# Kernel optimization log

Measured on AMD Instinct MI355X. Metric: run time of the kernel, lower is better.

Reference implementation:

```python
import jax, jax.numpy as jnp
import numpy as np

D_MODEL = 512
INF = 1e9
TEMP = np.sqrt(D_MODEL).astype(np.float32)


def setup_inputs() -> dict:
    key = jax.random.key(0)
    kq, kk, kv, km = jax.random.split(key, 4)
    B, L, D = 64, 1024, 64  # B = batch*heads
    q = jax.random.normal(kq, (B, L, D), dtype=jnp.float32)
    k = jax.random.normal(kk, (B, L, D), dtype=jnp.float32)
    v = jax.random.normal(kv, (B, L, D), dtype=jnp.float32)
    attn_mask = jax.random.randint(km, (B, L, L), 0, 2).astype(jnp.bool_)
    return {"q": q, "k": k, "v": v, "attn_mask": attn_mask}


def reference(q, k, v, attn_mask):
    # scores: [b, len_q, len_k]
    attn = jnp.einsum('bqd,bkd->bqk', q, k) / TEMP
    attn = jnp.where(attn_mask, -INF, attn)
    attn = jax.nn.softmax(attn, axis=2)
    # dropout p=0.0 -> identity
    out = jnp.einsum('bqk,bkd->bqd', attn, v)
    return out
```

## Files before the change

### kernel.cpp

```cpp
#include <hip/hip_runtime.h>
#include <hip/hip_bf16.h>


typedef __attribute__((ext_vector_type(4))) float f32x4;
typedef __attribute__((ext_vector_type(8))) short bf16x8;
typedef __attribute__((ext_vector_type(4))) short short4v;

constexpr int B_ = 64;
constexpr int L_ = 1024;
constexpr int D_ = 64;
constexpr int QBLK = 64;
constexpr int KV = 64;
constexpr int NKV = L_ / KV;
constexpr int STR = 72;
constexpr float INV_TEMP = 0.04419417382415922f;
constexpr float NEG = -1e9f;

__device__ inline short f2bf(float f) {
  __hip_bfloat16 h = __float2bfloat16(f);
  short s; __builtin_memcpy(&s, &h, 2);
  return s;
}

__global__ __launch_bounds__(256, 3) void attn_fwd(
    const float* __restrict__ Q, const float* __restrict__ K,
    const float* __restrict__ V, const int* __restrict__ M,
    float* __restrict__ O)
{
  __shared__ short k_lds[2][KV][STR];
  __shared__ short vt_lds[2][D_][STR];
  __shared__ short p_lds[4][16][STR];

  const int tid  = threadIdx.x;
  const int w    = tid >> 6;
  const int lane = tid & 63;
  const int g    = lane >> 4;
  const int c    = lane & 15;

  const int p   = blockIdx.x;
  const int xcd = p & 7;
  const int j   = p >> 3;
  const int b   = xcd + 8 * (j >> 4);
  const int q0  = (j & 15) * QBLK;

  bf16x8 qf[2];
  {
    const float* qp = Q + ((size_t)b * L_ + q0 + w * 16 + c) * D_ + g * 8;
#pragma unroll
    for (int ks = 0; ks < 2; ++ks) {
      f32x4 x0 = *(const f32x4*)(qp + ks * 32);
      f32x4 x1 = *(const f32x4*)(qp + ks * 32 + 4);
      bf16x8 t;
      t[0] = f2bf(x0[0] * INV_TEMP); t[1] = f2bf(x0[1] * INV_TEMP);
      t[2] = f2bf(x0[2] * INV_TEMP); t[3] = f2bf(x0[3] * INV_TEMP);
      t[4] = f2bf(x1[0] * INV_TEMP); t[5] = f2bf(x1[1] * INV_TEMP);
      t[6] = f2bf(x1[2] * INV_TEMP); t[7] = f2bf(x1[3] * INV_TEMP);
      qf[ks] = t;
    }
  }

  const float* Kb = K + (size_t)b * L_ * D_;
  const float* Vb = V + (size_t)b * L_ * D_;
  const int* mlane = M + (size_t)b * L_ * L_ + (size_t)(q0 + w * 16 + c) * L_ + 4 * g;

  f32x4 kreg[4], vreg[4];
  int4  mA[4], mB[4];
  const int vkey4 = (tid & 15) * 4;
  const int vd4   = (tid >> 4) * 4;

  auto load_kv = [&](int t) {
    const float* ksrc = Kb + (size_t)(t * KV) * D_;
    const float* vsrc = Vb + (size_t)(t * KV) * D_;
#pragma unroll
    for (int i = 0; i < 4; ++i) {
      kreg[i] = *(const f32x4*)(ksrc + (size_t)(tid + i * 256) * 4);
      vreg[i] = *(const f32x4*)(vsrc + (size_t)(vkey4 + i) * D_ + vd4);
    }
  };
  auto load_m = [&](int t, int4 (&mr)[4]) {
#pragma unroll
    for (int f = 0; f < 4; ++f) mr[f] = *(const int4*)(mlane + t * KV + f * 16);
  };
  auto write_kv = [&](int buf) {
#pragma unroll
    for (int i = 0; i < 4; ++i) {
      const int idx = tid + i * 256;
      short4v ks4 = { f2bf(kreg[i][0]), f2bf(kreg[i][1]),
                      f2bf(kreg[i][2]), f2bf(kreg[i][3]) };
      *(short4v*)&k_lds[buf][idx >> 4][(idx & 15) * 4] = ks4;
      const int jj = (i + (tid >> 4)) & 3;
      short4v vt4 = { f2bf(vreg[0][jj]), f2bf(vreg[1][jj]),
                      f2bf(vreg[2][jj]), f2bf(vreg[3][jj]) };
      *(short4v*)&vt_lds[buf][vd4 + jj][vkey4] = vt4;
    }
  };

  f32x4 acc[4];
#pragma unroll
  for (int i = 0; i < 4; ++i) acc[i] = (f32x4){0.f, 0.f, 0.f, 0.f};
  float m_run = -INFINITY;
  float l_run = 0.f;

  load_kv(0);
  write_kv(0);
  load_m(0, mA);
  load_m(1, mB);
  __syncthreads();

  auto body = [&](int t, int4 (&mbuf)[4], bool refill) {
    const int cur = t & 1;
    const bool has_next = (t + 1 < NKV);
    if (has_next) load_kv(t + 1);
    int4 mc[4];
#pragma unroll
    for (int f = 0; f < 4; ++f) mc[f] = mbuf[f];
    if (refill) load_m(t + 2, mbuf);
    __builtin_amdgcn_sched_barrier(0);

    f32x4 sc[4];
#pragma unroll
    for (int f = 0; f < 4; ++f) {
      const int4 mm = mc[f];
      sc[f][0] = mm.x ? NEG : 0.0f;
      sc[f][1] = mm.y ? NEG : 0.0f;
      sc[f][2] = mm.z ? NEG : 0.0f;
      sc[f][3] = mm.w ? NEG : 0.0f;
    }

#pragma unroll
    for (int f = 0; f < 4; ++f) {
      f32x4 a = sc[f];
#pragma unroll
      for (int ks = 0; ks < 2; ++ks) {
        bf16x8 kf = *(const bf16x8*)&k_lds[cur][f * 16 + c][ks * 32 + g * 8];
        a = __builtin_amdgcn_mfma_f32_16x16x32_bf16(kf, qf[ks], a, 0, 0, 0);
      }
      sc[f] = a;
    }

    float x = sc[0][0];
#pragma unroll
    for (int f = 0; f < 4; ++f)
#pragma unroll
      for (int r = 0; r < 4; ++r) x = fmaxf(x, sc[f][r]);
    x = fmaxf(x, __shfl_xor(x, 16, 64));
    x = fmaxf(x, __shfl_xor(x, 32, 64));
    const float m_new = fmaxf(m_run, x);
    const float alpha = __expf(m_run - m_new);
    float s = 0.f;
#pragma unroll
    for (int f = 0; f < 4; ++f)
#pragma unroll
      for (int r = 0; r < 4; ++r) {
        sc[f][r] = __expf(sc[f][r] - m_new);
        s += sc[f][r];
      }
    s += __shfl_xor(s, 16, 64);
    s += __shfl_xor(s, 32, 64);
    l_run = l_run * alpha + s;
    m_run = m_new;

    float ar[4];
#pragma unroll
    for (int r = 0; r < 4; ++r)
      ar[r] = __shfl(alpha, (lane & 48) | (g * 4 + r), 64);
#pragma unroll
    for (int fd = 0; fd < 4; ++fd)
#pragma unroll
      for (int r = 0; r < 4; ++r) acc[fd][r] *= ar[r];

#pragma unroll
    for (int f = 0; f < 4; ++f) {
      short4v pk = { f2bf(sc[f][0]), f2bf(sc[f][1]),
                     f2bf(sc[f][2]), f2bf(sc[f][3]) };
      *(short4v*)&p_lds[w][c][f * 16 + 4 * g] = pk;
    }

#pragma unroll
    for (int ks = 0; ks < 2; ++ks) {
      bf16x8 pa = *(const bf16x8*)&p_lds[w][c][ks * 32 + g * 8];
#pragma unroll
      for (int fd = 0; fd < 4; ++fd) {
        bf16x8 vb = *(const bf16x8*)&vt_lds[cur][fd * 16 + c][ks * 32 + g * 8];
        acc[fd] = __builtin_amdgcn_mfma_f32_16x16x32_bf16(pa, vb, acc[fd], 0, 0, 0);
      }
    }

    if (has_next) write_kv(cur ^ 1);
    __syncthreads();
  };

  for (int tt = 0; tt < NKV; tt += 2) {
    body(tt,     mA, tt + 2 < NKV);
    body(tt + 1, mB, tt + 3 < NKV);
  }

  const float li = 1.0f / l_run;
  float lr[4];
#pragma unroll
  for (int r = 0; r < 4; ++r)
    lr[r] = __shfl(li, (lane & 48) | (g * 4 + r), 64);
  float* orow = O + ((size_t)b * L_ + q0 + w * 16 + g * 4) * D_;
#pragma unroll
  for (int fd = 0; fd < 4; ++fd)
#pragma unroll
    for (int r = 0; r < 4; ++r)
      orow[(size_t)r * D_ + fd * 16 + c] = acc[fd][r] * lr[r];
}

extern "C" void kernel_launch(void* const* d_in, const int* in_sizes, int n_in,
                              void* d_out, int out_size, void* d_ws, size_t ws_size,
                              hipStream_t stream) {
  const float* q = (const float*)d_in[0];
  const float* k = (const float*)d_in[1];
  const float* v = (const float*)d_in[2];
  const int* m = (const int*)d_in[3];
  float* o = (float*)d_out;
  attn_fwd<<<dim3(1024), 256, 0, stream>>>(q, k, v, m, o);
}
```

Measured before the change: 98.75 us.

## Make each wave load its own K/V tiles, removing block-wide LDS sharing and barriers

Each of the four waves now reads K directly from global memory into registers as bf16 MFMA fragments, and transposes its own full copy of the V tile into a private LDS region. The shared double-buffered K/V LDS staging and the per-iteration __syncthreads are removed, so waves no longer wait on one another. In exchange, every wave reads the whole K/V tile itself, which quadruples global/L2 traffic and conversion work. The loads are no longer prefetched one tile ahead, so their latency is exposed inside each iteration.

```diff
diff --git a/kernel.cpp b/kernel.cpp
--- a/kernel.cpp
+++ b/kernel.cpp
@@ -27,8 +27,7 @@
     const float* __restrict__ V, const int* __restrict__ M,
     float* __restrict__ O)
 {
-  __shared__ short k_lds[2][KV][STR];
-  __shared__ short vt_lds[2][D_][STR];
+  __shared__ short vt_lds[4][D_][STR];
   __shared__ short p_lds[4][16][STR];
 
   const int tid  = threadIdx.x;
@@ -42,6 +41,9 @@
   const int j   = p >> 3;
   const int b   = xcd + 8 * (j >> 4);
   const int q0  = (j & 15) * QBLK;
+
+  short (*vt)[STR] = vt_lds[w];
+  short (*pl)[STR] = p_lds[w];
 
   bf16x8 qf[2];
   {
@@ -63,36 +65,10 @@
   const float* Vb = V + (size_t)b * L_ * D_;
   const int* mlane = M + (size_t)b * L_ * L_ + (size_t)(q0 + w * 16 + c) * L_ + 4 * g;
 
-  f32x4 kreg[4], vreg[4];
-  int4  mA[4], mB[4];
-  const int vkey4 = (tid & 15) * 4;
-  const int vd4   = (tid >> 4) * 4;
-
-  auto load_kv = [&](int t) {
-    const float* ksrc = Kb + (size_t)(t * KV) * D_;
-    const float* vsrc = Vb + (size_t)(t * KV) * D_;
-#pragma unroll
-    for (int i = 0; i < 4; ++i) {
-      kreg[i] = *(const f32x4*)(ksrc + (size_t)(tid + i * 256) * 4);
-      vreg[i] = *(const f32x4*)(vsrc + (size_t)(vkey4 + i) * D_ + vd4);
-    }
-  };
+  int4 mA[4], mB[4];
   auto load_m = [&](int t, int4 (&mr)[4]) {
 #pragma unroll
     for (int f = 0; f < 4; ++f) mr[f] = *(const int4*)(mlane + t * KV + f * 16);
-  };
-  auto write_kv = [&](int buf) {
-#pragma unroll
-    for (int i = 0; i < 4; ++i) {
-      const int idx = tid + i * 256;
-      short4v ks4 = { f2bf(kreg[i][0]), f2bf(kreg[i][1]),
-                      f2bf(kreg[i][2]), f2bf(kreg[i][3]) };
-      *(short4v*)&k_lds[buf][idx >> 4][(idx & 15) * 4] = ks4;
-      const int jj = (i + (tid >> 4)) & 3;
-      short4v vt4 = { f2bf(vreg[0][jj]), f2bf(vreg[1][jj]),
-                      f2bf(vreg[2][jj]), f2bf(vreg[3][jj]) };
-      *(short4v*)&vt_lds[buf][vd4 + jj][vkey4] = vt4;
-    }
   };
 
   f32x4 acc[4];
@@ -101,42 +77,57 @@
   float m_run = -INFINITY;
   float l_run = 0.f;
 
-  load_kv(0);
-  write_kv(0);
   load_m(0, mA);
   load_m(1, mB);
-  __syncthreads();
 
   auto body = [&](int t, int4 (&mbuf)[4], bool refill) {
-    const int cur = t & 1;
-    const bool has_next = (t + 1 < NKV);
-    if (has_next) load_kv(t + 1);
     int4 mc[4];
 #pragma unroll
     for (int f = 0; f < 4; ++f) mc[f] = mbuf[f];
     if (refill) load_m(t + 2, mbuf);
-    __builtin_amdgcn_sched_barrier(0);
+
+    f32x4 vreg[4][4];
+#pragma unroll
+    for (int ii = 0; ii < 4; ++ii)
+#pragma unroll
+      for (int i = 0; i < 4; ++i)
+        vreg[ii][i] = *(const f32x4*)(Vb + (size_t)(t * KV + g * 4 + 16 * ii + i) * D_ + c * 4);
+
+    bf16x8 kf[4][2];
+#pragma unroll
+    for (int f = 0; f < 4; ++f)
+#pragma unroll
+      for (int ks = 0; ks < 2; ++ks) {
+        const float* kp = Kb + (size_t)(t * KV + f * 16 + c) * D_ + ks * 32 + g * 8;
+        f32x4 x0 = *(const f32x4*)kp;
+        f32x4 x1 = *(const f32x4*)(kp + 4);
+        bf16x8 kk;
+        kk[0] = f2bf(x0[0]); kk[1] = f2bf(x0[1]); kk[2] = f2bf(x0[2]); kk[3] = f2bf(x0[3]);
+        kk[4] = f2bf(x1[0]); kk[5] = f2bf(x1[1]); kk[6] = f2bf(x1[2]); kk[7] = f2bf(x1[3]);
+        kf[f][ks] = kk;
+      }
 
     f32x4 sc[4];
 #pragma unroll
     for (int f = 0; f < 4; ++f) {
-      const int4 mm = mc[f];
-      sc[f][0] = mm.x ? NEG : 0.0f;
-      sc[f][1] = mm.y ? NEG : 0.0f;
-      sc[f][2] = mm.z ? NEG : 0.0f;
-      sc[f][3] = mm.w ? NEG : 0.0f;
-    }
-
-#pragma unroll
-    for (int f = 0; f < 4; ++f) {
-      f32x4 a = sc[f];
-#pragma unroll
-      for (int ks = 0; ks < 2; ++ks) {
-        bf16x8 kf = *(const bf16x8*)&k_lds[cur][f * 16 + c][ks * 32 + g * 8];
-        a = __builtin_amdgcn_mfma_f32_16x16x32_bf16(kf, qf[ks], a, 0, 0, 0);
-      }
+      f32x4 a;
+      a[0] = mc[f].x ? NEG : 0.0f;
+      a[1] = mc[f].y ? NEG : 0.0f;
+      a[2] = mc[f].z ? NEG : 0.0f;
+      a[3] = mc[f].w ? NEG : 0.0f;
+      a = __builtin_amdgcn_mfma_f32_16x16x32_bf16(kf[f][0], qf[0], a, 0, 0, 0);
+      a = __builtin_amdgcn_mfma_f32_16x16x32_bf16(kf[f][1], qf[1], a, 0, 0, 0);
       sc[f] = a;
     }
+
+#pragma unroll
+    for (int ii = 0; ii < 4; ++ii)
+#pragma unroll
+      for (int jj = 0; jj < 4; ++jj) {
+        short4v vt4 = { f2bf(vreg[ii][0][jj]), f2bf(vreg[ii][1][jj]),
+                        f2bf(vreg[ii][2][jj]), f2bf(vreg[ii][3][jj]) };
+        *(short4v*)&vt[c * 4 + jj][g * 4 + 16 * ii] = vt4;
+      }
 
     float x = sc[0][0];
 #pragma unroll
@@ -173,21 +164,18 @@
     for (int f = 0; f < 4; ++f) {
       short4v pk = { f2bf(sc[f][0]), f2bf(sc[f][1]),
                      f2bf(sc[f][2]), f2bf(sc[f][3]) };
-      *(short4v*)&p_lds[w][c][f * 16 + 4 * g] = pk;
+      *(short4v*)&pl[c][f * 16 + 4 * g] = pk;
     }
 
 #pragma unroll
     for (int ks = 0; ks < 2; ++ks) {
-      bf16x8 pa = *(const bf16x8*)&p_lds[w][c][ks * 32 + g * 8];
+      bf16x8 pa = *(const bf16x8*)&pl[c][ks * 32 + g * 8];
 #pragma unroll
       for (int fd = 0; fd < 4; ++fd) {
-        bf16x8 vb = *(const bf16x8*)&vt_lds[cur][fd * 16 + c][ks * 32 + g * 8];
+        bf16x8 vb = *(const bf16x8*)&vt[fd * 16 + c][ks * 32 + g * 8];
         acc[fd] = __builtin_amdgcn_mfma_f32_16x16x32_bf16(pa, vb, acc[fd], 0, 0, 0);
       }
     }
-
-    if (has_next) write_kv(cur ^ 1);
-    __syncthreads();
   };
 
   for (int tt = 0; tt < NKV; tt += 2) {
```

After: 274.6 us. 2.78x slower.

## Double query block to 128 rows and split K/V staging across wave halves

Applied to the files above, without the earlier changes.

Doubles the query tile per workgroup to 128 rows using 8 waves (512 threads), halving the grid so each staged K/V tile is reused by twice as many query rows. K/V staging is split so the first 256 threads load and convert K and the other 256 load and transpose V, cutting per-thread staging registers. This reduces redundant K/V global reads and conversions. In exchange there are fewer workgroups (512) for the CUs, and barriers now span 8 waves. The mask stream, which dominates bandwidth, is unchanged.

```diff
diff --git a/kernel.cpp b/kernel.cpp
--- a/kernel.cpp
+++ b/kernel.cpp
@@ -9,7 +9,7 @@
 constexpr int B_ = 64;
 constexpr int L_ = 1024;
 constexpr int D_ = 64;
-constexpr int QBLK = 64;
+constexpr int QBLK = 128;
 constexpr int KV = 64;
 constexpr int NKV = L_ / KV;
 constexpr int STR = 72;
@@ -22,14 +22,14 @@
   return s;
 }
 
-__global__ __launch_bounds__(256, 3) void attn_fwd(
+__global__ __launch_bounds__(512, 4) void attn_fwd(
     const float* __restrict__ Q, const float* __restrict__ K,
     const float* __restrict__ V, const int* __restrict__ M,
     float* __restrict__ O)
 {
   __shared__ short k_lds[2][KV][STR];
   __shared__ short vt_lds[2][D_][STR];
-  __shared__ short p_lds[4][16][STR];
+  __shared__ short p_lds[8][16][STR];
 
   const int tid  = threadIdx.x;
   const int w    = tid >> 6;
@@ -40,8 +40,8 @@
   const int p   = blockIdx.x;
   const int xcd = p & 7;
   const int j   = p >> 3;
-  const int b   = xcd + 8 * (j >> 4);
-  const int q0  = (j & 15) * QBLK;
+  const int b   = xcd + 8 * (j >> 3);
+  const int q0  = (j & 7) * QBLK;
 
   bf16x8 qf[2];
   {
@@ -63,18 +63,25 @@
   const float* Vb = V + (size_t)b * L_ * D_;
   const int* mlane = M + (size_t)b * L_ * L_ + (size_t)(q0 + w * 16 + c) * L_ + 4 * g;
 
-  f32x4 kreg[4], vreg[4];
+  const bool kstager = (tid < 256);
+  const int  htid    = tid & 255;
+  const int  vkey4   = (htid & 15) * 4;
+  const int  vd4     = (htid >> 4) * 4;
+
+  f32x4 sreg[4];
   int4  mA[4], mB[4];
-  const int vkey4 = (tid & 15) * 4;
-  const int vd4   = (tid >> 4) * 4;
 
   auto load_kv = [&](int t) {
-    const float* ksrc = Kb + (size_t)(t * KV) * D_;
-    const float* vsrc = Vb + (size_t)(t * KV) * D_;
-#pragma unroll
-    for (int i = 0; i < 4; ++i) {
-      kreg[i] = *(const f32x4*)(ksrc + (size_t)(tid + i * 256) * 4);
-      vreg[i] = *(const f32x4*)(vsrc + (size_t)(vkey4 + i) * D_ + vd4);
+    if (kstager) {
+      const float* ksrc = Kb + (size_t)(t * KV) * D_;
+#pragma unroll
+      for (int i = 0; i < 4; ++i)
+        sreg[i] = *(const f32x4*)(ksrc + (size_t)(htid + i * 256) * 4);
+    } else {
+      const float* vsrc = Vb + (size_t)(t * KV) * D_;
+#pragma unroll
+      for (int i = 0; i < 4; ++i)
+        sreg[i] = *(const f32x4*)(vsrc + (size_t)(vkey4 + i) * D_ + vd4);
     }
   };
   auto load_m = [&](int t, int4 (&mr)[4]) {
@@ -82,16 +89,22 @@
     for (int f = 0; f < 4; ++f) mr[f] = *(const int4*)(mlane + t * KV + f * 16);
   };
   auto write_kv = [&](int buf) {
-#pragma unroll
-    for (int i = 0; i < 4; ++i) {
-      const int idx = tid + i * 256;
-      short4v ks4 = { f2bf(kreg[i][0]), f2bf(kreg[i][1]),
-                      f2bf(kreg[i][2]), f2bf(kreg[i][3]) };
-      *(short4v*)&k_lds[buf][idx >> 4][(idx & 15) * 4] = ks4;
-      const int jj = (i + (tid >> 4)) & 3;
-      short4v vt4 = { f2bf(vreg[0][jj]), f2bf(vreg[1][jj]),
-                      f2bf(vreg[2][jj]), f2bf(vreg[3][jj]) };
-      *(short4v*)&vt_lds[buf][vd4 + jj][vkey4] = vt4;
+    if (kstager) {
+#pragma unroll
+      for (int i = 0; i < 4; ++i) {
+        const int idx = htid + i * 256;
+        short4v ks4 = { f2bf(sreg[i][0]), f2bf(sreg[i][1]),
+                        f2bf(sreg[i][2]), f2bf(sreg[i][3]) };
+        *(short4v*)&k_lds[buf][idx >> 4][(idx & 15) * 4] = ks4;
+      }
+    } else {
+#pragma unroll
+      for (int i = 0; i < 4; ++i) {
+        const int jj = (i + (htid >> 4)) & 3;
+        short4v vt4 = { f2bf(sreg[0][jj]), f2bf(sreg[1][jj]),
+                        f2bf(sreg[2][jj]), f2bf(sreg[3][jj]) };
+        *(short4v*)&vt_lds[buf][vd4 + jj][vkey4] = vt4;
+      }
     }
   };
 
@@ -120,11 +133,10 @@
     f32x4 sc[4];
 #pragma unroll
     for (int f = 0; f < 4; ++f) {
-      const int4 mm = mc[f];
-      sc[f][0] = mm.x ? NEG : 0.0f;
-      sc[f][1] = mm.y ? NEG : 0.0f;
-      sc[f][2] = mm.z ? NEG : 0.0f;
-      sc[f][3] = mm.w ? NEG : 0.0f;
+      sc[f][0] = mc[f].x ? NEG : 0.0f;
+      sc[f][1] = mc[f].y ? NEG : 0.0f;
+      sc[f][2] = mc[f].z ? NEG : 0.0f;
+      sc[f][3] = mc[f].w ? NEG : 0.0f;
     }
 
 #pragma unroll
@@ -216,5 +228,5 @@
   const float* v = (const float*)d_in[2];
   const int* m = (const int*)d_in[3];
   float* o = (float*)d_out;
-  attn_fwd<<<dim3(1024), 256, 0, stream>>>(q, k, v, m, o);
+  attn_fwd<<<dim3(512), 512, 0, stream>>>(q, k, v, m, o);
 }
```

New measurement: 116.4 us. +17.9%, slower.

## Single-buffer K/V LDS tiles and raise occupancy target to four blocks

Applied to the files above, without the earlier changes.

Replaces the double-buffered K and V^T shared-memory tiles with single buffers, which shrinks LDS per block. It also raises the launch-bounds minimum from 3 to 4 blocks per CU so more waves can be resident. The cost is an extra __syncthreads before each LDS refill, so writing the next tile no longer overlaps with other waves still reading the current one. Tighter register limits from the new launch bound may also cause spills.

```diff
diff --git a/kernel.cpp b/kernel.cpp
--- a/kernel.cpp
+++ b/kernel.cpp
@@ -22,13 +22,13 @@
   return s;
 }
 
-__global__ __launch_bounds__(256, 3) void attn_fwd(
+__global__ __launch_bounds__(256, 4) void attn_fwd(
     const float* __restrict__ Q, const float* __restrict__ K,
     const float* __restrict__ V, const int* __restrict__ M,
     float* __restrict__ O)
 {
-  __shared__ short k_lds[2][KV][STR];
-  __shared__ short vt_lds[2][D_][STR];
+  __shared__ short k_lds[KV][STR];
+  __shared__ short vt_lds[D_][STR];
   __shared__ short p_lds[4][16][STR];
 
   const int tid  = threadIdx.x;
@@ -81,17 +81,17 @@
 #pragma unroll
     for (int f = 0; f < 4; ++f) mr[f] = *(const int4*)(mlane + t * KV + f * 16);
   };
-  auto write_kv = [&](int buf) {
+  auto write_kv = [&]() {
 #pragma unroll
     for (int i = 0; i < 4; ++i) {
       const int idx = tid + i * 256;
       short4v ks4 = { f2bf(kreg[i][0]), f2bf(kreg[i][1]),
                       f2bf(kreg[i][2]), f2bf(kreg[i][3]) };
-      *(short4v*)&k_lds[buf][idx >> 4][(idx & 15) * 4] = ks4;
+      *(short4v*)&k_lds[idx >> 4][(idx & 15) * 4] = ks4;
       const int jj = (i + (tid >> 4)) & 3;
       short4v vt4 = { f2bf(vreg[0][jj]), f2bf(vreg[1][jj]),
                       f2bf(vreg[2][jj]), f2bf(vreg[3][jj]) };
-      *(short4v*)&vt_lds[buf][vd4 + jj][vkey4] = vt4;
+      *(short4v*)&vt_lds[vd4 + jj][vkey4] = vt4;
     }
   };
 
@@ -102,13 +102,12 @@
   float l_run = 0.f;
 
   load_kv(0);
-  write_kv(0);
+  write_kv();
   load_m(0, mA);
   load_m(1, mB);
   __syncthreads();
 
   auto body = [&](int t, int4 (&mbuf)[4], bool refill) {
-    const int cur = t & 1;
     const bool has_next = (t + 1 < NKV);
     if (has_next) load_kv(t + 1);
     int4 mc[4];
@@ -120,11 +119,10 @@
     f32x4 sc[4];
 #pragma unroll
     for (int f = 0; f < 4; ++f) {
-      const int4 mm = mc[f];
-      sc[f][0] = mm.x ? NEG : 0.0f;
-      sc[f][1] = mm.y ? NEG : 0.0f;
-      sc[f][2] = mm.z ? NEG : 0.0f;
-      sc[f][3] = mm.w ? NEG : 0.0f;
+      sc[f][0] = mc[f].x ? NEG : 0.0f;
+      sc[f][1] = mc[f].y ? NEG : 0.0f;
+      sc[f][2] = mc[f].z ? NEG : 0.0f;
+      sc[f][3] = mc[f].w ? NEG : 0.0f;
     }
 
 #pragma unroll
@@ -132,7 +130,7 @@
       f32x4 a = sc[f];
 #pragma unroll
       for (int ks = 0; ks < 2; ++ks) {
-        bf16x8 kf = *(const bf16x8*)&k_lds[cur][f * 16 + c][ks * 32 + g * 8];
+        bf16x8 kf = *(const bf16x8*)&k_lds[f * 16 + c][ks * 32 + g * 8];
         a = __builtin_amdgcn_mfma_f32_16x16x32_bf16(kf, qf[ks], a, 0, 0, 0);
       }
       sc[f] = a;
@@ -181,13 +179,16 @@
       bf16x8 pa = *(const bf16x8*)&p_lds[w][c][ks * 32 + g * 8];
 #pragma unroll
       for (int fd = 0; fd < 4; ++fd) {
-        bf16x8 vb = *(const bf16x8*)&vt_lds[cur][fd * 16 + c][ks * 32 + g * 8];
+        bf16x8 vb = *(const bf16x8*)&vt_lds[fd * 16 + c][ks * 32 + g * 8];
         acc[fd] = __builtin_amdgcn_mfma_f32_16x16x32_bf16(pa, vb, acc[fd], 0, 0, 0);
       }
     }
 
-    if (has_next) write_kv(cur ^ 1);
-    __syncthreads();
+    if (has_next) {
+      __syncthreads();
+      write_kv();
+      __syncthreads();
+    }
   };
 
   for (int tt = 0; tt < NKV; tt += 2) {
```

After: 199.9 us. 102% more time.
